# Optimization experiments

Hardware: AMD Instinct MI355X
Metric: run time of the kernel (lower is better)

Reference implementation:

```python
import jax, jax.numpy as jnp
import numpy as np
from functools import partial

N_SEEDS = 1000       # n
BG_LOW, BG_UP = 0.3, 0.7
ERODE_K, ERODE_ITER = 11, 1
KSZ = 3
IGNORE = -255
INT_MAX = np.iinfo(np.int32).max


def _min_pool2d(x, k):
    # binary erosion with a kxk all-ones structuring element, SAME padding
    return jax.lax.reduce_window(x, INT_MAX, jax.lax.min, (k, k), (1, 1), 'SAME')


def _max_pool3d(x, k):
    # binary dilation over (B,H,W) with kxk window on spatial dims
    return jax.lax.reduce_window(x, -INT_MAX, jax.lax.max, (1, k, k), (1, 1, 1), 'SAME')


def _otsu_threshold(flat255):
    # flat255: int32 pixel values in [0,255]
    hist = jnp.zeros(256, jnp.float32).at[flat255].add(1.0)
    total = jnp.asarray(flat255.shape[0], jnp.float32)
    bins = jnp.arange(256, dtype=jnp.float32)
    w = jnp.cumsum(hist)                 # class-0 pixel count up to bin t
    m = jnp.cumsum(hist * bins)          # class-0 intensity mass up to t
    mT = m[-1]
    denom = w * (total - w)
    sigma_b = jnp.where(denom > 0, (mT * w - total * m) ** 2 / (denom * total * total), 0.0)
    th = jnp.argmax(sigma_b).astype(jnp.float32)
    bad = jnp.sum(hist > 0) <= 1         # degenerate histogram -> bad_egg
    return th, bad


def _sample_mask(eligible, key, hw):
    # uniform sampling without replacement of min(N_SEEDS, #eligible)
    # via random-score top-k restricted to eligible positions
    scores = jnp.where(eligible, jax.random.uniform(key, (hw,)), -jnp.inf)
    vals, idx = jax.lax.top_k(scores, N_SEEDS)
    sel = (vals > -jnp.inf).astype(jnp.int32)
    return jnp.zeros(hw, jnp.int32).at[idx].max(sel)


def _one_sample(cam, key):
    h, w = cam.shape
    hw = h * w
    cam255 = jnp.floor(cam * 255.0)
    flat255 = jnp.clip(cam255.astype(jnp.int32).ravel(), 0, 255)

    th, bad = _otsu_threshold(flat255)
    th = jnp.where(bad, jnp.median(cam * 255.0), th)
    th = jnp.where(th == 0, 1.0, jnp.where(th == 255, 254.0, th))

    roi = (cam255 > th).astype(jnp.int32)
    for _ in range(ERODE_ITER):
        roi = _min_pool2d(roi, ERODE_K)

    kf, kb, kz = jax.random.split(key, 3)
    # foreground: sample uniformly from eroded ROI pixels
    fg = _sample_mask(roi.ravel() == 1, kf, hw)
    # background: sample uniformly from the nbr_bg lowest-activation pixels
    z = jax.random.uniform(kz, (), minval=BG_LOW, maxval=BG_UP)
    nbr_bg = jnp.ceil(z * hw)
    order = jnp.argsort(cam.ravel())
    rank = jnp.zeros(hw, jnp.int32).at[order].set(jnp.arange(hw, dtype=jnp.int32))
    bg = _sample_mask(rank.astype(jnp.float32) < nbr_bg, kb, hw)
    return fg.reshape(h, w), bg.reshape(h, w)


def setup_inputs() -> dict:
    key = jax.random.key(0)
    x = jax.random.uniform(key, (128, 1, 512, 512), dtype=jnp.float32)
    return {"x": x}


def reference(x):
    b, d, h, w = x.shape
    keys = jax.random.split(jax.random.key(42), b)
    all_fg, all_bg = jax.vmap(_one_sample)(x[:, 0], keys)   # (B,H,W) int32
    # dilation with ksz x ksz ones kernel
    all_fg = _max_pool3d(all_fg, KSZ)
    all_bg = _max_pool3d(all_bg, KSZ)
    outer = all_fg + all_bg
    all_fg = jnp.where(outer == 2, 0, all_fg)
    all_bg = jnp.where(outer == 2, 0, all_bg)
    out = jnp.full((b, h, w), IGNORE, dtype=jnp.int32)
    out = jnp.where(all_fg == 1, 1, out)
    out = jnp.where(all_bg == 1, 0, out)
    return out
```

## Files before the change

kernel.cpp:

```cpp
#include <hip/hip_runtime.h>
#include <cstdint>

typedef unsigned short u16;

constexpr int BATCH = 128;
constexpr int H = 512, W = 512;
constexpr int HW = H * W;
constexpr int WPR = W / 64;
constexpr int WPI = HW / 64;
constexpr int NSEED = 1000;
constexpr int MARGIN = 3000;
constexpr int CAP2 = 4096;
constexpr int CAPS = 1024;
constexpr int LBUF = 2048;
constexpr int NBIN = 4096;
constexpr int QSEG = 256;

__device__ __forceinline__ uint32_t rotl32(uint32_t v, int d) {
  return (v << d) | (v >> (32 - d));
}

__device__ __forceinline__ void tf2x32(uint32_t k0, uint32_t k1,
                                       uint32_t x0, uint32_t x1,
                                       uint32_t &o0, uint32_t &o1) {
  uint32_t ks2 = k0 ^ k1 ^ 0x1BD11BDAu;
  x0 += k0; x1 += k1;
  x0 += x1; x1 = rotl32(x1, 13); x1 ^= x0;
  x0 += x1; x1 = rotl32(x1, 15); x1 ^= x0;
  x0 += x1; x1 = rotl32(x1, 26); x1 ^= x0;
  x0 += x1; x1 = rotl32(x1, 6);  x1 ^= x0;
  x0 += k1; x1 += ks2 + 1u;
  x0 += x1; x1 = rotl32(x1, 17); x1 ^= x0;
  x0 += x1; x1 = rotl32(x1, 29); x1 ^= x0;
  x0 += x1; x1 = rotl32(x1, 16); x1 ^= x0;
  x0 += x1; x1 = rotl32(x1, 24); x1 ^= x0;
  x0 += ks2; x1 += k0 + 2u;
  x0 += x1; x1 = rotl32(x1, 13); x1 ^= x0;
  x0 += x1; x1 = rotl32(x1, 15); x1 ^= x0;
  x0 += x1; x1 = rotl32(x1, 26); x1 ^= x0;
  x0 += x1; x1 = rotl32(x1, 6);  x1 ^= x0;
  x0 += k0; x1 += k1 + 3u;
  x0 += x1; x1 = rotl32(x1, 17); x1 ^= x0;
  x0 += x1; x1 = rotl32(x1, 29); x1 ^= x0;
  x0 += x1; x1 = rotl32(x1, 16); x1 ^= x0;
  x0 += x1; x1 = rotl32(x1, 24); x1 ^= x0;
  x0 += k1; x1 += ks2 + 4u;
  x0 += x1; x1 = rotl32(x1, 13); x1 ^= x0;
  x0 += x1; x1 = rotl32(x1, 15); x1 ^= x0;
  x0 += x1; x1 = rotl32(x1, 26); x1 ^= x0;
  x0 += x1; x1 = rotl32(x1, 6);  x1 ^= x0;
  x0 += ks2; x1 += k0 + 5u;
  o0 = x0; o1 = x1;
}

__device__ __forceinline__ uint32_t score_bits(uint32_t k0, uint32_t k1, uint32_t i) {
  uint32_t a, c; tf2x32(k0, k1, 0u, i, a, c);
  return a ^ c;
}

__device__ __forceinline__ void keygen(int b, uint32_t* keys, uint32_t* kbg,
                                       uint32_t* Tbg) {
  uint32_t kb0, kb1; tf2x32(0u, 42u, 0u, (uint32_t)b, kb0, kb1);
  uint32_t kf0, kf1; tf2x32(kb0, kb1, 0u, 0u, kf0, kf1);
  uint32_t kB0, kB1; tf2x32(kb0, kb1, 0u, 1u, kB0, kB1);
  uint32_t kz0, kz1; tf2x32(kb0, kb1, 0u, 2u, kz0, kz1);
  uint32_t za, zc; tf2x32(kz0, kz1, 0u, 0u, za, zc);
  uint32_t zb = za ^ zc;
  keys[b * 4 + 0] = kf0; keys[b * 4 + 1] = kf1;
  keys[b * 4 + 2] = kB0; keys[b * 4 + 3] = kB1;
  float uu = __uint_as_float((zb >> 9) | 0x3f800000u) - 1.0f;
  float span = __fsub_rn(0.7f, 0.3f);
  float z = __fadd_rn(__fmul_rn(uu, span), 0.3f);
  z = fmaxf(0.3f, z);
  float nb = ceilf(__fmul_rn(z, (float)HW));
  uint32_t K = (uint32_t)nb;
  kbg[b] = K;
  float tv = floorf((1.0f - (float)MARGIN / (float)K) * 8388608.0f);
  Tbg[b] = (uint32_t)fmaxf(tv, 0.0f);
}

__global__ __launch_bounds__(1024) void k_binify(const float4* __restrict__ x4,
                                                 u16* __restrict__ g,
                                                 uint32_t* __restrict__ gh,
                                                 uint32_t* __restrict__ keys,
                                                 uint32_t* __restrict__ kbg,
                                                 uint32_t* __restrict__ Tbg,
                                                 uint32_t* __restrict__ Efg,
                                                 uint32_t* __restrict__ cnt_fg,
                                                 uint32_t* __restrict__ cnt_be,
                                                 uint32_t* __restrict__ cnt_bg) {
  __shared__ uint32_t h[NBIN];
  int b = blockIdx.x >> 2, sub = blockIdx.x & 3, t = threadIdx.x;
  if (blockIdx.x == 0 && t < BATCH) {
    keygen(t, keys, kbg, Tbg);
    Efg[t] = 0; cnt_be[t] = 0; cnt_bg[t] = 0;
  }
  if (blockIdx.x == 0 && t < 2 * BATCH) cnt_fg[t] = 0;
  for (int i = t; i < NBIN; i += 1024) h[i] = 0;
  __syncthreads();
  const float4* xb = x4 + ((size_t)b * HW + (size_t)sub * (HW / 4)) / 4;
  ushort4* gb4 = (ushort4*)g + ((size_t)b * HW + (size_t)sub * (HW / 4)) / 4;
  for (int i = t; i < HW / 16; i += 1024) {
    float4 v4 = xb[i];
    int g0 = (int)floorf(__fmul_rn(v4.x, 4080.0f)); g0 = min(max(g0, 0), 4079);
    int g1 = (int)floorf(__fmul_rn(v4.y, 4080.0f)); g1 = min(max(g1, 0), 4079);
    int g2 = (int)floorf(__fmul_rn(v4.z, 4080.0f)); g2 = min(max(g2, 0), 4079);
    int g3 = (int)floorf(__fmul_rn(v4.w, 4080.0f)); g3 = min(max(g3, 0), 4079);
    atomicAdd(&h[g0], 1u);
    atomicAdd(&h[g1], 1u);
    atomicAdd(&h[g2], 1u);
    atomicAdd(&h[g3], 1u);
    ushort4 o;
    o.x = (u16)g0; o.y = (u16)g1; o.z = (u16)g2; o.w = (u16)g3;
    gb4[i] = o;
  }
  __syncthreads();
  uint32_t* dst = gh + ((size_t)blockIdx.x << 12);
  for (int i = t; i < NBIN; i += 1024) dst[i] = h[i];
}

__device__ __forceinline__ void lds_tree_cumsum256x2(float* Lc, float* Sc,
                                                     float* Lm, float* Sm, int tid) {
  const int off[9] = {0, 256, 384, 448, 480, 496, 504, 508, 510};
  const int sz[9]  = {256, 128, 64, 32, 16, 8, 4, 2, 1};
  for (int l = 0; l < 8; ++l) {
    int o = off[l], on = off[l + 1], n = sz[l + 1];
    if (tid < n) {
      Lc[on + tid] = __fadd_rn(Lc[o + 2 * tid], Lc[o + 2 * tid + 1]);
      Lm[on + tid] = __fadd_rn(Lm[o + 2 * tid], Lm[o + 2 * tid + 1]);
    }
    __syncthreads();
  }
  if (tid == 0) { Sc[off[8]] = Lc[off[8]]; Sm[off[8]] = Lm[off[8]]; }
  __syncthreads();
  for (int l = 7; l >= 0; --l) {
    int o = off[l], on = off[l + 1], hn = sz[l] / 2;
    if (tid == 0) { Sc[o] = Lc[o]; Sm[o] = Lm[o]; }
    if (tid < hn) { Sc[o + 2 * tid + 1] = Sc[on + tid]; Sm[o + 2 * tid + 1] = Sm[on + tid]; }
    if (tid >= 1 && tid < hn) {
      Sc[o + 2 * tid] = __fadd_rn(Sc[on + tid - 1], Lc[o + 2 * tid]);
      Sm[o + 2 * tid] = __fadd_rn(Sm[on + tid - 1], Lm[o + 2 * tid]);
    }
    __syncthreads();
  }
}

__global__ __launch_bounds__(256) void k_otsu(const uint32_t* __restrict__ gh,
                                              const uint32_t* __restrict__ kbg,
                                              int* __restrict__ th_out,
                                              uint32_t* __restrict__ b1a,
                                              uint32_t* __restrict__ r1a) {
  __shared__ uint32_t h[NBIN];
  __shared__ float Lc[511], Sc[511], Lm[511], Sm[511];
  __shared__ float av[4];
  __shared__ int ai[4];
  int b = blockIdx.x, t = threadIdx.x;
  const uint32_t* g0 = gh + ((size_t)(b * 4 + 0) << 12);
  const uint32_t* g1 = gh + ((size_t)(b * 4 + 1) << 12);
  const uint32_t* g2 = gh + ((size_t)(b * 4 + 2) << 12);
  const uint32_t* g3 = gh + ((size_t)(b * 4 + 3) << 12);
  for (int i = t; i < NBIN; i += 256) h[i] = g0[i] + g1[i] + g2[i] + g3[i];
  __syncthreads();
  uint32_t hv = 0;
#pragma unroll
  for (int i = 0; i < 16; ++i) hv += h[t * 16 + ((i + t) & 15)];
  Lc[t] = (float)hv;
  Lm[t] = __fmul_rn((float)hv, (float)t);
  __syncthreads();
  lds_tree_cumsum256x2(Lc, Sc, Lm, Sm, t);
  uint32_t K = kbg[b];
  {
    float total = (float)HW;
    float mT = Sm[255];
    float w = Sc[t];
    float denom = __fmul_rn(w, __fsub_rn(total, w));
    float s = 0.0f;
    if (denom > 0.0f) {
      float d  = __fsub_rn(__fmul_rn(mT, w), __fmul_rn(total, Sm[t]));
      float nu = __fmul_rn(d, d);
      float dd = __fmul_rn(__fmul_rn(denom, total), total);
      s = __fdiv_rn(nu, dd);
    }
    float bv = s; int bidx = t;
#pragma unroll
    for (int d = 32; d >= 1; d >>= 1) {
      float ov = __shfl_xor(bv, d, 64);
      int oi = __shfl_xor(bidx, d, 64);
      if (ov > bv || (ov == bv && oi < bidx)) { bv = ov; bidx = oi; }
    }
    if ((t & 63) == 0) { av[t >> 6] = bv; ai[t >> 6] = bidx; }
    bool gf = (Sc[t] >= (float)K) && (t == 0 || Sc[t - 1] < (float)K);
    if (gf) {
      uint32_t accv = (t == 0) ? 0u : (uint32_t)Sc[t - 1];
      uint32_t b1v = 0, r1v = 1;
      for (int bin = t * 16; bin < t * 16 + 16; ++bin) {
        uint32_t cc = h[bin];
        if (accv + cc >= K) { b1v = (uint32_t)bin; r1v = K - accv; break; }
        accv += cc;
      }
      b1a[b] = b1v; r1a[b] = r1v;
    }
  }
  __syncthreads();
  if (t == 0) {
    float bv = av[0]; int bidx = ai[0];
#pragma unroll
    for (int wv = 1; wv < 4; ++wv) {
      float ov = av[wv]; int oi = ai[wv];
      if (ov > bv || (ov == bv && oi < bidx)) { bv = ov; bidx = oi; }
    }
    int bi = bidx;
    if (bi == 0) bi = 1;
    if (bi == 255) bi = 254;
    th_out[b] = bi;
  }
}

__global__ __launch_bounds__(1024) void k_main(const u16* __restrict__ gq,
                                               const float* __restrict__ x,
                                               const int* __restrict__ th,
                                               const uint32_t* __restrict__ b1a,
                                               const uint32_t* __restrict__ Tbg,
                                               const uint32_t* __restrict__ keys,
                                               uint32_t* __restrict__ Efg,
                                               uint32_t* __restrict__ cnt_bg,
                                               uint64_t* __restrict__ list,
                                               uint32_t* __restrict__ cnt_be,
                                               uint64_t* __restrict__ list_be,
                                               uint64_t* __restrict__ erod) {
  __shared__ uint64_t sroi[1104];
  __shared__ uint64_t srow[1104];
  __shared__ uint64_t lbuf[LBUF];
  __shared__ uint32_t wq[16 * QSEG];
  __shared__ uint32_t lcnt, gbase;
  int b = blockIdx.x >> 2, sub = blockIdx.x & 3, t = threadIdx.x;
  int wave = t >> 6, lane = t & 63;
  int R0 = sub * 128;
  int rlo = max(R0 - 5, 0), rhi = min(R0 + 133, H);
  int nwords = (rhi - rlo) * 8;
  const u16* gb = gq + (size_t)b * HW;
  const float* xb = x + (size_t)b * HW;
  int groi = (th[b] + 1) << 4;
  uint32_t b1 = b1a[b];
  uint32_t T = Tbg[b];
  uint32_t k0 = keys[b * 4 + 2], k1 = keys[b * 4 + 3];
  if (t == 0) lcnt = 0;
  __syncthreads();
  uint32_t* q = wq + wave * QSEG;
  uint32_t qlen = 0, hd = 0;
  uint64_t lmask = (1ull << lane) - 1ull;
  for (int r = 0; r < 8; ++r) {
    int absr = R0 + wave * 8 + r;
    int rowbase = absr * W + lane;
    int swbase = (absr - rlo) * 8;
    const u16* gp8 = gb + rowbase;
    u16 gvals[8];
#pragma unroll
    for (int c = 0; c < 8; ++c) gvals[c] = gp8[c * 64];
#pragma unroll
    for (int c = 0; c < 8; ++c) {
      uint32_t gv = (uint32_t)gvals[c];
      uint64_t bw = __ballot((int)gv >= groi);
      if (lane == 0) sroi[swbase + c] = bw;
      bool elig = gv < b1;
      uint64_t m = __ballot(elig);
      if (elig) {
        uint32_t rank = (uint32_t)__popcll(m & lmask);
        uint32_t idx = hd + qlen + rank;
        if (idx >= (uint32_t)QSEG) idx -= (uint32_t)QSEG;
        q[idx] = (uint32_t)(rowbase + c * 64);
      }
      qlen += (uint32_t)__popcll(m);
      if (gv == b1) {
        uint32_t gp = atomicAdd(&cnt_be[b], 1u);
        if (gp < (uint32_t)CAPS)
          list_be[(size_t)b * CAPS + gp] =
              (((uint64_t)__float_as_uint(xb[rowbase + c * 64])) << 18) |
              (uint32_t)(rowbase + c * 64);
      }
      while (qlen >= 128u) {
        __builtin_amdgcn_wave_barrier();
        uint32_t i0 = hd + (uint32_t)lane;
        if (i0 >= (uint32_t)QSEG) i0 -= (uint32_t)QSEG;
        uint32_t i1 = hd + 64u + (uint32_t)lane;
        if (i1 >= (uint32_t)QSEG) i1 -= (uint32_t)QSEG;
        uint32_t p0 = q[i0];
        uint32_t p1 = q[i1];
        hd += 128u; if (hd >= (uint32_t)QSEG) hd -= (uint32_t)QSEG;
        qlen -= 128u;
        uint32_t v0 = score_bits(k0, k1, p0) >> 9;
        uint32_t v1 = score_bits(k0, k1, p1) >> 9;
        if (v0 >= T) {
          uint32_t pos = atomicAdd(&lcnt, 1u);
          uint64_t key = (((uint64_t)((~v0) & 0x7FFFFFu)) << 18) | p0;
          if (pos < (uint32_t)LBUF) lbuf[pos] = key;
          else { uint32_t gp = atomicAdd(&cnt_bg[b], 1u);
                 if (gp < (uint32_t)CAP2) list[(size_t)b * CAP2 + gp] = key; }
        }
        if (v1 >= T) {
          uint32_t pos = atomicAdd(&lcnt, 1u);
          uint64_t key = (((uint64_t)((~v1) & 0x7FFFFFu)) << 18) | p1;
          if (pos < (uint32_t)LBUF) lbuf[pos] = key;
          else { uint32_t gp = atomicAdd(&cnt_bg[b], 1u);
                 if (gp < (uint32_t)CAP2) list[(size_t)b * CAP2 + gp] = key; }
        }
      }
    }
  }
  while (qlen >= 64u) {
    __builtin_amdgcn_wave_barrier();
    uint32_t idx = hd + (uint32_t)lane;
    if (idx >= (uint32_t)QSEG) idx -= (uint32_t)QSEG;
    uint32_t p = q[idx];
    hd += 64u; if (hd >= (uint32_t)QSEG) hd -= (uint32_t)QSEG;
    qlen -= 64u;
    uint32_t v = score_bits(k0, k1, p) >> 9;
    if (v >= T) {
      uint32_t pos = atomicAdd(&lcnt, 1u);
      uint64_t key = (((uint64_t)((~v) & 0x7FFFFFu)) << 18) | p;
      if (pos < (uint32_t)LBUF) lbuf[pos] = key;
      else { uint32_t gp = atomicAdd(&cnt_bg[b], 1u);
             if (gp < (uint32_t)CAP2) list[(size_t)b * CAP2 + gp] = key; }
    }
  }
  if (qlen) {
    __builtin_amdgcn_wave_barrier();
    if ((uint32_t)lane < qlen) {
      uint32_t idx = hd + (uint32_t)lane;
      if (idx >= (uint32_t)QSEG) idx -= (uint32_t)QSEG;
      uint32_t p = q[idx];
      uint32_t v = score_bits(k0, k1, p) >> 9;
      if (v >= T) {
        uint32_t pos = atomicAdd(&lcnt, 1u);
        uint64_t key = (((uint64_t)((~v) & 0x7FFFFFu)) << 18) | p;
        if (pos < (uint32_t)LBUF) lbuf[pos] = key;
        else { uint32_t gp = atomicAdd(&cnt_bg[b], 1u);
               if (gp < (uint32_t)CAP2) list[(size_t)b * CAP2 + gp] = key; }
      }
    }
  }
  {
    int lowWords = (R0 - rlo) * 8;
    int nh = nwords - 1024;
    for (int i = wave; i < nh; i += 16) {
      int wi = i + ((i < lowWords) ? 0 : 1024);
      int absr = rlo + (wi >> 3);
      int c = wi & 7;
      uint32_t gv = (uint32_t)gb[absr * W + c * 64 + lane];
      uint64_t bw = __ballot((int)gv >= groi);
      if (lane == 0) sroi[wi] = bw;
    }
  }
  __syncthreads();
  for (int wi = t; wi < nwords; wi += 1024) {
    int c = wi & 7;
    uint64_t cur = sroi[wi];
    uint64_t left  = (c > 0) ? sroi[wi - 1] : ~0ull;
    uint64_t right = (c < 7) ? sroi[wi + 1] : ~0ull;
    uint64_t res = cur;
#pragma unroll
    for (int s = 1; s <= 5; ++s) {
      res &= (cur >> s) | (right << (64 - s));
      res &= (cur << s) | (left >> (64 - s));
    }
    srow[wi] = res;
  }
  __syncthreads();
  {
    int coreRow = t >> 3, c = t & 7;
    int absr = R0 + coreRow;
    int s = absr - rlo;
    uint64_t res = srow[s * 8 + c];
#pragma unroll
    for (int d = 1; d <= 5; ++d) {
      if (absr - d >= 0) res &= srow[(s - d) * 8 + c];
      if (absr + d < H)  res &= srow[(s + d) * 8 + c];
    }
    erod[(size_t)b * WPI + absr * 8 + c] = res;
    uint32_t pc = (uint32_t)__popcll(res);
    for (int sh = 32; sh >= 1; sh >>= 1) pc += __shfl_down(pc, sh);
    if (lane == 0 && pc) atomicAdd(&Efg[b], pc);
  }
  __syncthreads();
  int m = min((int)lcnt, LBUF);
  if (t == 0) gbase = atomicAdd(&cnt_bg[b], (uint32_t)m);
  __syncthreads();
  uint32_t base = gbase;
  for (int i = t; i < m; i += 1024) {
    uint32_t pos = base + (uint32_t)i;
    if (pos < (uint32_t)CAP2) list[(size_t)b * CAP2 + pos] = lbuf[i];
  }
}

__global__ __launch_bounds__(1024) void k_selcomp(const uint32_t* __restrict__ r1a,
                                                  const uint32_t* __restrict__ cnt_be,
                                                  const uint64_t* __restrict__ list_be,
                                                  const uint32_t* __restrict__ Tbg,
                                                  const uint32_t* __restrict__ keys,
                                                  const uint32_t* __restrict__ cnt_bg,
                                                  const uint64_t* __restrict__ list,
                                                  const uint32_t* __restrict__ Ea,
                                                  uint32_t* __restrict__ cnt_fg,
                                                  uint64_t* __restrict__ list_fg,
                                                  const uint64_t* __restrict__ bmE,
                                                  int* __restrict__ out) {
  __shared__ uint64_t Gbit[WPI];
  __shared__ uint64_t Fbit[WPI];
  __shared__ uint64_t pool[5248];
  __shared__ uint32_t ecnt, tcnt, lcnt, gbase, sb2, sr2;
  int b = blockIdx.x >> 1, sub = blockIdx.x & 1, t = threadIdx.x;
  int bsub = b * 2 + sub;
  uint32_t* G32 = (uint32_t*)Gbit;
  uint32_t* F32 = (uint32_t*)Fbit;
  uint32_t* h = (uint32_t*)(pool + 2048);
  uint64_t* tie = pool + 4096;
  uint32_t* S = (uint32_t*)(pool + 5120);
  for (int i = t; i < WPI; i += 1024) { Gbit[i] = 0; Fbit[i] = 0; }
  if (t == 0) { ecnt = 0; tcnt = 0; }

  {
    uint64_t* ks = pool;
    uint64_t* ebuf = pool + 1024;
    int nbe = min((int)cnt_be[b], CAPS);
    if (t < nbe) ks[t] = list_be[(size_t)b * CAPS + t];
    __syncthreads();
    if (t < nbe) {
      uint64_t mk = ks[t];
      int rank = 0;
      for (int i = 0; i < nbe; ++i) rank += (ks[i] < mk) ? 1 : 0;
      int r = min((int)r1a[b], nbe);
      if (rank < r) {
        uint32_t p = (uint32_t)(mk & 0x3FFFFull);
        uint32_t v = score_bits(keys[b * 4 + 2], keys[b * 4 + 3], p) >> 9;
        if (v >= Tbg[b]) {
          uint32_t slot = atomicAdd(&ecnt, 1u);
          ebuf[slot] = (((uint64_t)((~v) & 0x7FFFFFu)) << 18) | p;
        }
      }
    }
    for (int i = t; i < 4096; i += 1024) h[i] = 0;
    __syncthreads();
    int n0 = min((int)cnt_bg[b], CAP2);
    int ne = (int)ecnt;
    int n = n0 + ne;
    if (n > 0) {
      uint32_t target = (uint32_t)min(NSEED, n);
      const uint64_t* lb = list + (size_t)b * CAP2;
      uint64_t K0 = (t < n0)        ? lb[t]        : 0;
      uint64_t K1 = (t + 1024 < n0) ? lb[t + 1024] : 0;
      uint64_t K2 = (t + 2048 < n0) ? lb[t + 2048] : 0;
      uint64_t K3 = (t + 3072 < n0) ? lb[t + 3072] : 0;
      uint64_t KE = (t < ne)        ? ebuf[t]      : 0;
      if (t < n0)        atomicAdd(&h[(uint32_t)(K0 >> 29)], 1u);
      if (t + 1024 < n0) atomicAdd(&h[(uint32_t)(K1 >> 29)], 1u);
      if (t + 2048 < n0) atomicAdd(&h[(uint32_t)(K2 >> 29)], 1u);
      if (t + 3072 < n0) atomicAdd(&h[(uint32_t)(K3 >> 29)], 1u);
      if (t < ne)        atomicAdd(&h[(uint32_t)(KE >> 29)], 1u);
      __syncthreads();
      if (t < 256) {
        uint32_t s = 0;
#pragma unroll
        for (int i = 0; i < 16; ++i) s += h[t * 16 + ((i + t) & 15)];
        S[t] = s;
      }
      __syncthreads();
      for (int st = 1; st < 256; st <<= 1) {
        uint32_t v = 0;
        if (t < 256 && t >= st) v = S[t - st];
        __syncthreads();
        if (t < 256) S[t] += v;
        __syncthreads();
      }
      if (t < 256) {
        uint32_t before = (t == 0) ? 0u : S[t - 1];
        if (S[t] >= target && before < target) {
          uint32_t acc = before;
          for (int i = 0; i < 16; ++i) {
            uint32_t c = h[t * 16 + i];
            if (acc + c >= target) { sb2 = (uint32_t)(t * 16 + i); sr2 = target - acc; break; }
            acc += c;
          }
        }
      }
      __syncthreads();
      uint32_t b2 = sb2, r2 = sr2;
#define PROCB(KK, VALID) \
      if (VALID) { \
        uint32_t bin = (uint32_t)((KK) >> 29); \
        if (bin < b2) { \
          uint32_t p = (uint32_t)(KK) & 0x3FFFFu; \
          atomicOr(&G32[p >> 5], 1u << (p & 31)); \
        } else if (bin == b2) { \
          uint32_t pos = atomicAdd(&tcnt, 1u); \
          if (pos < 1024u) tie[pos] = (KK); \
        } \
      }
      PROCB(K0, t < n0) PROCB(K1, t + 1024 < n0) PROCB(K2, t + 2048 < n0)
      PROCB(K3, t + 3072 < n0) PROCB(KE, t < ne)
#undef PROCB
      __syncthreads();
      int m = min((int)tcnt, 1024);
      int r = min((int)r2, m);
      if (t < m) {
        uint64_t mk = tie[t];
        int rank = 0;
        for (int i = 0; i < m; ++i) rank += (tie[i] < mk) ? 1 : 0;
        if (rank < r) {
          uint32_t p = (uint32_t)mk & 0x3FFFFu;
          atomicOr(&G32[p >> 5], 1u << (p & 31));
        }
      }
    }
  }
  __syncthreads();

  {
    uint32_t E = Ea[b];
    const uint64_t* eb = bmE + (size_t)b * WPI;
    if (E <= (uint32_t)NSEED) {
      for (int i = t; i < WPI; i += 1024) Fbit[i] = eb[i];
      __syncthreads();
    } else {
      uint64_t* lbuf = pool;
      if (t == 0) { lcnt = 0; tcnt = 0; }
      for (int i = t; i < 4096; i += 1024) h[i] = 0;
      __syncthreads();
      float tvf = floorf((1.0f - (float)MARGIN / (float)E) * 8388608.0f);
      uint32_t T = (uint32_t)fmaxf(tvf, 0.0f);
      uint32_t k0 = keys[b * 4 + 0], k1 = keys[b * 4 + 1];
      int lane = t & 63;
      for (int k = 0; k < HW / 1024; ++k) {
        uint32_t p = (uint32_t)(k * 1024 + t);
        uint64_t wbits = eb[p >> 6];
        if ((wbits >> lane) & 1ull) {
          uint32_t v = score_bits(k0, k1, p) >> 9;
          if (v >= T) {
            uint32_t pos = atomicAdd(&lcnt, 1u);
            uint64_t key = (((uint64_t)((~v) & 0x7FFFFFu)) << 18) | p;
            if (pos < (uint32_t)LBUF) lbuf[pos] = key;
            else { uint32_t gp = atomicAdd(&cnt_fg[bsub], 1u);
                   if (gp < (uint32_t)CAP2) list_fg[(size_t)bsub * CAP2 + gp] = key; }
          }
        }
      }
      __syncthreads();
      int m2 = min((int)lcnt, LBUF);
      if (t == 0) gbase = atomicAdd(&cnt_fg[bsub], (uint32_t)m2);
      __syncthreads();
      for (int i = t; i < m2; i += 1024) {
        uint32_t pos = gbase + (uint32_t)i;
        if (pos < (uint32_t)CAP2) list_fg[(size_t)bsub * CAP2 + pos] = lbuf[i];
      }
      __syncthreads();
      int n = min((int)cnt_fg[bsub], CAP2);
      if (n > 0) {
        uint32_t target = (uint32_t)min(NSEED, n);
        const uint64_t* lb = list_fg + (size_t)bsub * CAP2;
        uint64_t K0 = (t < n)        ? lb[t]        : 0;
        uint64_t K1 = (t + 1024 < n) ? lb[t + 1024] : 0;
        uint64_t K2 = (t + 2048 < n) ? lb[t + 2048] : 0;
        uint64_t K3 = (t + 3072 < n) ? lb[t + 3072] : 0;
        if (t < n)        atomicAdd(&h[(uint32_t)(K0 >> 29)], 1u);
        if (t + 1024 < n) atomicAdd(&h[(uint32_t)(K1 >> 29)], 1u);
        if (t + 2048 < n) atomicAdd(&h[(uint32_t)(K2 >> 29)], 1u);
        if (t + 3072 < n) atomicAdd(&h[(uint32_t)(K3 >> 29)], 1u);
        __syncthreads();
        if (t < 256) {
          uint32_t s = 0;
#pragma unroll
          for (int i = 0; i < 16; ++i) s += h[t * 16 + ((i + t) & 15)];
          S[t] = s;
        }
        __syncthreads();
        for (int st = 1; st < 256; st <<= 1) {
          uint32_t v = 0;
          if (t < 256 && t >= st) v = S[t - st];
          __syncthreads();
          if (t < 256) S[t] += v;
          __syncthreads();
        }
        if (t < 256) {
          uint32_t before = (t == 0) ? 0u : S[t - 1];
          if (S[t] >= target && before < target) {
            uint32_t acc = before;
            for (int i = 0; i < 16; ++i) {
              uint32_t c = h[t * 16 + i];
              if (acc + c >= target) { sb2 = (uint32_t)(t * 16 + i); sr2 = target - acc; break; }
              acc += c;
            }
          }
        }
        __syncthreads();
        uint32_t b2 = sb2, r2 = sr2;
#define PROCF(KK, VALID) \
        if (VALID) { \
          uint32_t bin = (uint32_t)((KK) >> 29); \
          if (bin < b2) { \
            uint32_t p = (uint32_t)(KK) & 0x3FFFFu; \
            atomicOr(&F32[p >> 5], 1u << (p & 31)); \
          } else if (bin == b2) { \
            uint32_t pos = atomicAdd(&tcnt, 1u); \
            if (pos < 1024u) tie[pos] = (KK); \
          } \
        }
        PROCF(K0, t < n) PROCF(K1, t + 1024 < n) PROCF(K2, t + 2048 < n)
        PROCF(K3, t + 3072 < n)
#undef PROCF
        __syncthreads();
        int m = min((int)tcnt, 1024);
        int r = min((int)r2, m);
        if (t < m) {
          uint64_t mk = tie[t];
          int rank = 0;
          for (int i = 0; i < m; ++i) rank += (tie[i] < mk) ? 1 : 0;
          if (rank < r) {
            uint32_t p = (uint32_t)mk & 0x3FFFFu;
            atomicOr(&F32[p >> 5], 1u << (p & 31));
          }
        }
      }
      __syncthreads();
    }
  }
  __syncthreads();

  uint64_t* FdS = pool;
  uint64_t* BdS = pool + 512;
  for (int it = 0; it < 4; ++it) {
    {
      int s = t >> 7, xx = t & 127;
      int w = xx & 63;
      int rg = sub * 32 + it * 8 + s;
      int r = rg * 8 + (w >> 3), c = w & 7;
      const uint64_t* src = (xx < 64) ? Fbit : Gbit;
      uint64_t d = 0;
#pragma unroll
      for (int dr = -1; dr <= 1; ++dr) {
        int rr = r + dr;
        if (rr < 0 || rr >= H) continue;
        int wi = rr * 8 + c;
        uint64_t cur = src[wi];
        uint64_t lf = (c > 0) ? src[wi - 1] : 0ull;
        uint64_t rt = (c < 7) ? src[wi + 1] : 0ull;
        d |= cur | (cur << 1) | (lf >> 63) | (cur >> 1) | (rt << 63);
      }
      if (xx < 64) FdS[s * 64 + w] = d; else BdS[s * 64 + w] = d;
    }
    __syncthreads();
    int4* ob = (int4*)out + (size_t)b * (HW / 4) + (size_t)sub * (HW / 8)
             + (size_t)it * 8192;
#pragma unroll
    for (int k2 = 0; k2 < 8; ++k2) {
      int idx = k2 * 1024 + t;
      int ss = idx >> 10, i = idx & 1023;
      int ww = i >> 4, sub4 = i & 15;
      uint64_t Fd = FdS[ss * 64 + ww], Bd = BdS[ss * 64 + ww];
      uint64_t ov = Fd & Bd;
      Fd &= ~ov; Bd &= ~ov;
      int sh = sub4 * 4;
      int4 o;
      o.x = ((Fd >> (sh + 0)) & 1ull) ? 1 : (((Bd >> (sh + 0)) & 1ull) ? 0 : -255);
      o.y = ((Fd >> (sh + 1)) & 1ull) ? 1 : (((Bd >> (sh + 1)) & 1ull) ? 0 : -255);
      o.z = ((Fd >> (sh + 2)) & 1ull) ? 1 : (((Bd >> (sh + 2)) & 1ull) ? 0 : -255);
      o.w = ((Fd >> (sh + 3)) & 1ull) ? 1 : (((Bd >> (sh + 3)) & 1ull) ? 0 : -255);
      ob[idx] = o;
    }
    __syncthreads();
  }
}

extern "C" void kernel_launch(void* const* d_in, const int* in_sizes, int n_in,
                              void* d_out, int out_size, void* d_ws, size_t ws_size,
                              hipStream_t stream) {
  (void)in_sizes; (void)n_in; (void)out_size; (void)ws_size;
  const float* x = (const float*)d_in[0];
  int* out = (int*)d_out;
  char* ws = (char*)d_ws;

  u16* g = (u16*)d_out;

  uint32_t* keys   = (uint32_t*)(ws + 0);
  uint32_t* kbg    = (uint32_t*)(ws + 2048);
  int*      th     = (int*)     (ws + 2560);
  uint32_t* b1a    = (uint32_t*)(ws + 3072);
  uint32_t* r1a    = (uint32_t*)(ws + 3584);
  uint32_t* Tbg    = (uint32_t*)(ws + 4096);
  uint32_t* Efg    = (uint32_t*)(ws + 4608);
  uint32_t* cnt_be = (uint32_t*)(ws + 5120);
  uint32_t* cnt_bg = (uint32_t*)(ws + 5632);
  uint32_t* cnt_fg = (uint32_t*)(ws + 6144);
  uint32_t* gh      = (uint32_t*)(ws + 8192);
  uint64_t* list    = (uint64_t*)(ws + 8192 + 8388608);
  uint64_t* list_be = (uint64_t*)(ws + 8192 + 8388608 + 4194304);
  uint64_t* bmE     = (uint64_t*)(ws + 8192 + 8388608 + 5242880);
  uint64_t* list_fg = (uint64_t*)gh;

  k_binify  <<<BATCH * 4, 1024, 0, stream>>>((const float4*)x, g, gh, keys, kbg,
                                             Tbg, Efg, cnt_fg, cnt_be, cnt_bg);
  k_otsu    <<<BATCH, 256, 0, stream>>>(gh, kbg, th, b1a, r1a);
  k_main    <<<BATCH * 4, 1024, 0, stream>>>(g, x, th, b1a, Tbg, keys,
                                             Efg, cnt_bg, list, cnt_be, list_be, bmE);
  k_selcomp <<<BATCH * 2, 1024, 0, stream>>>(r1a, cnt_be, list_be, Tbg, keys,
                                             cnt_bg, list, Efg, cnt_fg, list_fg,
                                             bmE, out);
}
```

Measured before the change: 335.6 us.

## Fuse Otsu into binify via last-block-done counter; prefetch rows; skip redundant clears

The Otsu threshold kernel is folded into the histogram kernel. The last of the four sub-blocks per image, detected with an atomic done counter and thread fences, merges the partial histograms and computes the threshold, so one kernel launch and its dependency gap disappear. Counter zeroing moves to a single memset on the host stream, and each image's keygen now runs in its own block. The main kernel prefetches the next row's bin values while processing the current row, and selcomp skips clearing Fbit when it will be overwritten. The cost is an extra memset launch and a serialized tail, since one block per image does the Otsu work.

```diff
diff --git a/kernel.cpp b/kernel.cpp
--- a/kernel.cpp
+++ b/kernel.cpp
@@ -79,23 +79,49 @@
   Tbg[b] = (uint32_t)fmaxf(tv, 0.0f);
 }
 
+__device__ __forceinline__ void lds_tree_cumsum256x2(float* Lc, float* Sc,
+                                                     float* Lm, float* Sm, int tid) {
+  const int off[9] = {0, 256, 384, 448, 480, 496, 504, 508, 510};
+  const int sz[9]  = {256, 128, 64, 32, 16, 8, 4, 2, 1};
+  for (int l = 0; l < 8; ++l) {
+    int o = off[l], on = off[l + 1], n = sz[l + 1];
+    if (tid < n) {
+      Lc[on + tid] = __fadd_rn(Lc[o + 2 * tid], Lc[o + 2 * tid + 1]);
+      Lm[on + tid] = __fadd_rn(Lm[o + 2 * tid], Lm[o + 2 * tid + 1]);
+    }
+    __syncthreads();
+  }
+  if (tid == 0) { Sc[off[8]] = Lc[off[8]]; Sm[off[8]] = Lm[off[8]]; }
+  __syncthreads();
+  for (int l = 7; l >= 0; --l) {
+    int o = off[l], on = off[l + 1], hn = sz[l] / 2;
+    if (tid == 0) { Sc[o] = Lc[o]; Sm[o] = Lm[o]; }
+    if (tid < hn) { Sc[o + 2 * tid + 1] = Sc[on + tid]; Sm[o + 2 * tid + 1] = Sm[on + tid]; }
+    if (tid >= 1 && tid < hn) {
+      Sc[o + 2 * tid] = __fadd_rn(Sc[on + tid - 1], Lc[o + 2 * tid]);
+      Sm[o + 2 * tid] = __fadd_rn(Sm[on + tid - 1], Lm[o + 2 * tid]);
+    }
+    __syncthreads();
+  }
+}
+
 __global__ __launch_bounds__(1024) void k_binify(const float4* __restrict__ x4,
                                                  u16* __restrict__ g,
                                                  uint32_t* __restrict__ gh,
                                                  uint32_t* __restrict__ keys,
                                                  uint32_t* __restrict__ kbg,
                                                  uint32_t* __restrict__ Tbg,
-                                                 uint32_t* __restrict__ Efg,
-                                                 uint32_t* __restrict__ cnt_fg,
-                                                 uint32_t* __restrict__ cnt_be,
-                                                 uint32_t* __restrict__ cnt_bg) {
+                                                 uint32_t* __restrict__ done,
+                                                 int* __restrict__ th_out,
+                                                 uint32_t* __restrict__ b1a,
+                                                 uint32_t* __restrict__ r1a) {
   __shared__ uint32_t h[NBIN];
+  __shared__ float Lc[511], Sc[511], Lm[511], Sm[511];
+  __shared__ float av[4];
+  __shared__ int ai[4];
+  __shared__ uint32_t amLast;
   int b = blockIdx.x >> 2, sub = blockIdx.x & 3, t = threadIdx.x;
-  if (blockIdx.x == 0 && t < BATCH) {
-    keygen(t, keys, kbg, Tbg);
-    Efg[t] = 0; cnt_be[t] = 0; cnt_bg[t] = 0;
-  }
-  if (blockIdx.x == 0 && t < 2 * BATCH) cnt_fg[t] = 0;
+  if (sub == 0 && t == 0) keygen(b, keys, kbg, Tbg);
   for (int i = t; i < NBIN; i += 1024) h[i] = 0;
   __syncthreads();
   const float4* xb = x4 + ((size_t)b * HW + (size_t)sub * (HW / 4)) / 4;
@@ -117,102 +143,74 @@
   __syncthreads();
   uint32_t* dst = gh + ((size_t)blockIdx.x << 12);
   for (int i = t; i < NBIN; i += 1024) dst[i] = h[i];
-}
-
-__device__ __forceinline__ void lds_tree_cumsum256x2(float* Lc, float* Sc,
-                                                     float* Lm, float* Sm, int tid) {
-  const int off[9] = {0, 256, 384, 448, 480, 496, 504, 508, 510};
-  const int sz[9]  = {256, 128, 64, 32, 16, 8, 4, 2, 1};
-  for (int l = 0; l < 8; ++l) {
-    int o = off[l], on = off[l + 1], n = sz[l + 1];
-    if (tid < n) {
-      Lc[on + tid] = __fadd_rn(Lc[o + 2 * tid], Lc[o + 2 * tid + 1]);
-      Lm[on + tid] = __fadd_rn(Lm[o + 2 * tid], Lm[o + 2 * tid + 1]);
-    }
-    __syncthreads();
-  }
-  if (tid == 0) { Sc[off[8]] = Lc[off[8]]; Sm[off[8]] = Lm[off[8]]; }
-  __syncthreads();
-  for (int l = 7; l >= 0; --l) {
-    int o = off[l], on = off[l + 1], hn = sz[l] / 2;
-    if (tid == 0) { Sc[o] = Lc[o]; Sm[o] = Lm[o]; }
-    if (tid < hn) { Sc[o + 2 * tid + 1] = Sc[on + tid]; Sm[o + 2 * tid + 1] = Sm[on + tid]; }
-    if (tid >= 1 && tid < hn) {
-      Sc[o + 2 * tid] = __fadd_rn(Sc[on + tid - 1], Lc[o + 2 * tid]);
-      Sm[o + 2 * tid] = __fadd_rn(Sm[on + tid - 1], Lm[o + 2 * tid]);
-    }
-    __syncthreads();
-  }
-}
-
-__global__ __launch_bounds__(256) void k_otsu(const uint32_t* __restrict__ gh,
-                                              const uint32_t* __restrict__ kbg,
-                                              int* __restrict__ th_out,
-                                              uint32_t* __restrict__ b1a,
-                                              uint32_t* __restrict__ r1a) {
-  __shared__ uint32_t h[NBIN];
-  __shared__ float Lc[511], Sc[511], Lm[511], Sm[511];
-  __shared__ float av[4];
-  __shared__ int ai[4];
-  int b = blockIdx.x, t = threadIdx.x;
-  const uint32_t* g0 = gh + ((size_t)(b * 4 + 0) << 12);
-  const uint32_t* g1 = gh + ((size_t)(b * 4 + 1) << 12);
-  const uint32_t* g2 = gh + ((size_t)(b * 4 + 2) << 12);
-  const uint32_t* g3 = gh + ((size_t)(b * 4 + 3) << 12);
-  for (int i = t; i < NBIN; i += 256) h[i] = g0[i] + g1[i] + g2[i] + g3[i];
-  __syncthreads();
-  uint32_t hv = 0;
-#pragma unroll
-  for (int i = 0; i < 16; ++i) hv += h[t * 16 + ((i + t) & 15)];
-  Lc[t] = (float)hv;
-  Lm[t] = __fmul_rn((float)hv, (float)t);
-  __syncthreads();
-  lds_tree_cumsum256x2(Lc, Sc, Lm, Sm, t);
-  uint32_t K = kbg[b];
+  __threadfence();
+  __syncthreads();
+  if (t == 0) amLast = (atomicAdd(&done[b], 1u) == 3u) ? 1u : 0u;
+  __syncthreads();
+  if (!amLast) return;
+  __threadfence();
   {
-    float total = (float)HW;
-    float mT = Sm[255];
-    float w = Sc[t];
-    float denom = __fmul_rn(w, __fsub_rn(total, w));
-    float s = 0.0f;
-    if (denom > 0.0f) {
-      float d  = __fsub_rn(__fmul_rn(mT, w), __fmul_rn(total, Sm[t]));
-      float nu = __fmul_rn(d, d);
-      float dd = __fmul_rn(__fmul_rn(denom, total), total);
-      s = __fdiv_rn(nu, dd);
-    }
-    float bv = s; int bidx = t;
-#pragma unroll
-    for (int d = 32; d >= 1; d >>= 1) {
-      float ov = __shfl_xor(bv, d, 64);
-      int oi = __shfl_xor(bidx, d, 64);
-      if (ov > bv || (ov == bv && oi < bidx)) { bv = ov; bidx = oi; }
-    }
-    if ((t & 63) == 0) { av[t >> 6] = bv; ai[t >> 6] = bidx; }
-    bool gf = (Sc[t] >= (float)K) && (t == 0 || Sc[t - 1] < (float)K);
-    if (gf) {
-      uint32_t accv = (t == 0) ? 0u : (uint32_t)Sc[t - 1];
-      uint32_t b1v = 0, r1v = 1;
-      for (int bin = t * 16; bin < t * 16 + 16; ++bin) {
-        uint32_t cc = h[bin];
-        if (accv + cc >= K) { b1v = (uint32_t)bin; r1v = K - accv; break; }
-        accv += cc;
-      }
-      b1a[b] = b1v; r1a[b] = r1v;
-    }
-  }
-  __syncthreads();
-  if (t == 0) {
-    float bv = av[0]; int bidx = ai[0];
-#pragma unroll
-    for (int wv = 1; wv < 4; ++wv) {
-      float ov = av[wv]; int oi = ai[wv];
-      if (ov > bv || (ov == bv && oi < bidx)) { bv = ov; bidx = oi; }
-    }
-    int bi = bidx;
-    if (bi == 0) bi = 1;
-    if (bi == 255) bi = 254;
-    th_out[b] = bi;
+    const uint32_t* g0 = gh + ((size_t)(b * 4 + 0) << 12);
+    const uint32_t* g1 = gh + ((size_t)(b * 4 + 1) << 12);
+    const uint32_t* g2 = gh + ((size_t)(b * 4 + 2) << 12);
+    const uint32_t* g3 = gh + ((size_t)(b * 4 + 3) << 12);
+    for (int i = t; i < NBIN; i += 1024) h[i] = g0[i] + g1[i] + g2[i] + g3[i];
+    __syncthreads();
+    if (t < 256) {
+      uint32_t hv = 0;
+#pragma unroll
+      for (int i = 0; i < 16; ++i) hv += h[t * 16 + ((i + t) & 15)];
+      Lc[t] = (float)hv;
+      Lm[t] = __fmul_rn((float)hv, (float)t);
+    }
+    __syncthreads();
+    lds_tree_cumsum256x2(Lc, Sc, Lm, Sm, t);
+    uint32_t K = kbg[b];
+    if (t < 256) {
+      float total = (float)HW;
+      float mT = Sm[255];
+      float w = Sc[t];
+      float denom = __fmul_rn(w, __fsub_rn(total, w));
+      float s = 0.0f;
+      if (denom > 0.0f) {
+        float d  = __fsub_rn(__fmul_rn(mT, w), __fmul_rn(total, Sm[t]));
+        float nu = __fmul_rn(d, d);
+        float dd = __fmul_rn(__fmul_rn(denom, total), total);
+        s = __fdiv_rn(nu, dd);
+      }
+      float bv = s; int bidx = t;
+#pragma unroll
+      for (int d = 32; d >= 1; d >>= 1) {
+        float ov = __shfl_xor(bv, d, 64);
+        int oi = __shfl_xor(bidx, d, 64);
+        if (ov > bv || (ov == bv && oi < bidx)) { bv = ov; bidx = oi; }
+      }
+      if ((t & 63) == 0) { av[t >> 6] = bv; ai[t >> 6] = bidx; }
+      bool gf = (Sc[t] >= (float)K) && (t == 0 || Sc[t - 1] < (float)K);
+      if (gf) {
+        uint32_t accv = (t == 0) ? 0u : (uint32_t)Sc[t - 1];
+        uint32_t b1v = 0, r1v = 1;
+        for (int bin = t * 16; bin < t * 16 + 16; ++bin) {
+          uint32_t cc = h[bin];
+          if (accv + cc >= K) { b1v = (uint32_t)bin; r1v = K - accv; break; }
+          accv += cc;
+        }
+        b1a[b] = b1v; r1a[b] = r1v;
+      }
+    }
+    __syncthreads();
+    if (t == 0) {
+      float bv = av[0]; int bidx = ai[0];
+#pragma unroll
+      for (int wv = 1; wv < 4; ++wv) {
+        float ov = av[wv]; int oi = ai[wv];
+        if (ov > bv || (ov == bv && oi < bidx)) { bv = ov; bidx = oi; }
+      }
+      int bi = bidx;
+      if (bi == 0) bi = 1;
+      if (bi == 255) bi = 254;
+      th_out[b] = bi;
+    }
   }
 }
 
@@ -249,14 +247,23 @@
   uint32_t* q = wq + wave * QSEG;
   uint32_t qlen = 0, hd = 0;
   uint64_t lmask = (1ull << lane) - 1ull;
+  int absr0 = R0 + wave * 8;
+  u16 gvals[8];
+  {
+    const u16* gp8 = gb + absr0 * W + lane;
+#pragma unroll
+    for (int c = 0; c < 8; ++c) gvals[c] = gp8[c * 64];
+  }
   for (int r = 0; r < 8; ++r) {
-    int absr = R0 + wave * 8 + r;
+    int absr = absr0 + r;
     int rowbase = absr * W + lane;
     int swbase = (absr - rlo) * 8;
-    const u16* gp8 = gb + rowbase;
-    u16 gvals[8];
-#pragma unroll
-    for (int c = 0; c < 8; ++c) gvals[c] = gp8[c * 64];
+    u16 gnext[8];
+    if (r < 7) {
+      const u16* gp8 = gb + (absr + 1) * W + lane;
+#pragma unroll
+      for (int c = 0; c < 8; ++c) gnext[c] = gp8[c * 64];
+    }
 #pragma unroll
     for (int c = 0; c < 8; ++c) {
       uint32_t gv = (uint32_t)gvals[c];
@@ -305,6 +312,10 @@
                  if (gp < (uint32_t)CAP2) list[(size_t)b * CAP2 + gp] = key; }
         }
       }
+    }
+    if (r < 7) {
+#pragma unroll
+      for (int c = 0; c < 8; ++c) gvals[c] = gnext[c];
     }
   }
   while (qlen >= 64u) {
@@ -415,7 +426,10 @@
   uint32_t* h = (uint32_t*)(pool + 2048);
   uint64_t* tie = pool + 4096;
   uint32_t* S = (uint32_t*)(pool + 5120);
-  for (int i = t; i < WPI; i += 1024) { Gbit[i] = 0; Fbit[i] = 0; }
+  uint32_t E = Ea[b];
+  for (int i = t; i < WPI; i += 1024) Gbit[i] = 0;
+  if (E > (uint32_t)NSEED)
+    for (int i = t; i < WPI; i += 1024) Fbit[i] = 0;
   if (t == 0) { ecnt = 0; tcnt = 0; }
 
   {
@@ -515,7 +529,6 @@
   __syncthreads();
 
   {
-    uint32_t E = Ea[b];
     const uint64_t* eb = bmE + (size_t)b * WPI;
     if (E <= (uint32_t)NSEED) {
       for (int i = t; i < WPI; i += 1024) Fbit[i] = eb[i];
@@ -689,15 +702,16 @@
   uint32_t* cnt_be = (uint32_t*)(ws + 5120);
   uint32_t* cnt_bg = (uint32_t*)(ws + 5632);
   uint32_t* cnt_fg = (uint32_t*)(ws + 6144);
+  uint32_t* done   = (uint32_t*)(ws + 7168);
   uint32_t* gh      = (uint32_t*)(ws + 8192);
   uint64_t* list    = (uint64_t*)(ws + 8192 + 8388608);
   uint64_t* list_be = (uint64_t*)(ws + 8192 + 8388608 + 4194304);
   uint64_t* bmE     = (uint64_t*)(ws + 8192 + 8388608 + 5242880);
   uint64_t* list_fg = (uint64_t*)gh;
 
+  hipMemsetAsync(ws + 4608, 0, 3072, stream);
   k_binify  <<<BATCH * 4, 1024, 0, stream>>>((const float4*)x, g, gh, keys, kbg,
-                                             Tbg, Efg, cnt_fg, cnt_be, cnt_bg);
-  k_otsu    <<<BATCH, 256, 0, stream>>>(gh, kbg, th, b1a, r1a);
+                                             Tbg, done, th, b1a, r1a);
   k_main    <<<BATCH * 4, 1024, 0, stream>>>(g, x, th, b1a, Tbg, keys,
                                              Efg, cnt_bg, list, cnt_be, list_be, bmE);
   k_selcomp <<<BATCH * 2, 1024, 0, stream>>>(r1a, cnt_be, list_be, Tbg, keys,
```

Result: slower. 601.3 us (+79.2%).
